# Performance work log

Hardware: AMD Instinct MI355X
Metric: run time of the kernel (lower is better)

Reference implementation:

```python
import jax, jax.numpy as jnp
import numpy as np

E = 500000
B = 1024
N_INC = 64
E_INC = 64
U_INC = 64
W_INC = 2
DIM_IN = E_INC + 2 * N_INC + U_INC          # 256
DIM_W2 = DIM_IN // 2                         # 128
DIM_X1 = DIM_IN + DIM_W2                     # 384
H1 = 256
H2 = 256
E_OUTC = 64
EPS = 1e-5


def _linear_params(key, d_in, d_out):
    kw, kb = jax.random.split(key)
    lim = 1.0 / np.sqrt(d_in)
    W = jax.random.uniform(kw, (d_in, d_out), minval=-lim, maxval=lim, dtype=jnp.float32)
    b = jax.random.uniform(kb, (d_out,), minval=-lim, maxval=lim, dtype=jnp.float32)
    return W, b


def setup_inputs() -> dict:
    key = jax.random.key(0)
    ks = jax.random.split(key, 12)
    src = jax.random.normal(ks[0], (E, N_INC), dtype=jnp.float32)
    dest = jax.random.normal(ks[1], (E, N_INC), dtype=jnp.float32)
    edge_attr = jax.random.normal(ks[2], (E, E_INC), dtype=jnp.float32)
    u = jax.random.normal(ks[3], (B, U_INC), dtype=jnp.float32)
    batch = jax.random.randint(ks[4], (E,), 0, B, dtype=jnp.int64)
    winding = jax.random.uniform(ks[5], (E, W_INC), dtype=jnp.float32)

    Ww, bw = _linear_params(ks[6], W_INC, DIM_W2)
    gw = jnp.ones((DIM_W2,), jnp.float32)
    betaw = jnp.zeros((DIM_W2,), jnp.float32)

    W1, b1 = _linear_params(ks[7], DIM_X1, H1)
    g1 = jnp.ones((H1,), jnp.float32)
    beta1 = jnp.zeros((H1,), jnp.float32)
    W2, b2 = _linear_params(ks[8], H1, H2)
    g2 = jnp.ones((H2,), jnp.float32)
    beta2 = jnp.zeros((H2,), jnp.float32)
    W3, b3 = _linear_params(ks[9], H2, E_OUTC)

    return {
        "src": src, "dest": dest, "edge_attr": edge_attr, "u": u,
        "batch": batch, "winding": winding,
        "Ww": Ww, "bw": bw, "gw": gw, "betaw": betaw,
        "W1": W1, "b1": b1, "g1": g1, "beta1": beta1,
        "W2": W2, "b2": b2, "g2": g2, "beta2": beta2,
        "W3": W3, "b3": b3,
    }


def _layernorm(x, g, b):
    mu = jnp.mean(x, axis=-1, keepdims=True)
    var = jnp.mean(jnp.square(x - mu), axis=-1, keepdims=True)
    return (x - mu) * jax.lax.rsqrt(var + EPS) * g + b


def reference(src, dest, edge_attr, u, batch, winding,
              Ww, bw, gw, betaw,
              W1, b1, g1, beta1,
              W2, b2, g2, beta2,
              W3, b3):
    # winding_mlp: Linear -> LayerNorm -> ReLU, [E, 2] -> [E, 128]
    w = jax.nn.relu(_layernorm(winding @ Ww + bw, gw, betaw))
    # gather per-graph features and concat: [E, 384]
    x = jnp.concatenate([src, dest, edge_attr, u[batch], w], axis=1)
    # mlp_h: (Linear -> LN -> ReLU) x2 -> Linear
    h = jax.nn.relu(_layernorm(x @ W1 + b1, g1, beta1))
    h = jax.nn.relu(_layernorm(h @ W2 + b2, g2, beta2))
    return h @ W3 + b3
```

## Files before the change

### kernel.cpp

```cpp
#include <hip/hip_runtime.h>
#include <stdint.h>

#define E_TOT 500000
#define BM 128
#define NTHREADS 512

typedef float f32x4 __attribute__((ext_vector_type(4)));
typedef short short8 __attribute__((ext_vector_type(8)));

__device__ __forceinline__ float b2f(ushort u) {
    union { uint32_t i; float f; } v; v.i = ((uint32_t)u) << 16; return v.f;
}
__device__ __forceinline__ ushort f2b(float f) {
    union { float f; uint32_t i; } v; v.f = f;
    uint32_t r = (v.i + 0x7FFFu + ((v.i >> 16) & 1u)) >> 16;
    return (ushort)r;
}
__device__ __forceinline__ float ldf(const void* p, int i, int f32m) {
    return f32m ? ((const float*)p)[i] : b2f(((const ushort*)p)[i]);
}

__global__ void detect_fmt(const void* src, const void* batch, int* flags) {
    __shared__ int s_ok, s_nz;
    if (threadIdx.x == 0) { s_ok = 0; s_nz = 0; }
    __syncthreads();
    int t = threadIdx.x;
    if (t < 64) {
        float f = fabsf(b2f(((const ushort*)src)[2 * t]));
        if (f > 1e-3f && f < 1e2f) atomicAdd(&s_ok, 1);
    }
    int hv = ((const int*)batch)[2 * t + 1];
    if (hv != 0) atomicOr(&s_nz, 1);
    __syncthreads();
    if (t == 0) { flags[0] = (s_ok < 32) ? 1 : 0; flags[1] = (s_nz == 0) ? 1 : 0; }
}

__global__ void prep(const int* __restrict__ flags,
                     const void* W1, const void* W2, const void* W3,
                     const void* Ww, const void* bw, const void* gw, const void* bew,
                     const void* b1, const void* g1, const void* be1,
                     const void* b2, const void* g2, const void* be2, const void* b3,
                     ushort* __restrict__ W1t, ushort* __restrict__ W2t,
                     ushort* __restrict__ W3t, float* __restrict__ params) {
    int f32m = flags[0];
    int id = blockIdx.x * 256 + threadIdx.x;
    if (id < 98304) {
        int n = id / 384, k = id - n * 384;
        W1t[id] = f2b(ldf(W1, k * 256 + n, f32m));
    } else if (id < 163840) {
        int t = id - 98304; int n = t >> 8, k = t & 255;
        W2t[t] = f2b(ldf(W2, k * 256 + n, f32m));
    } else if (id < 180224) {
        int t = id - 163840; int n = t >> 8, k = t & 255;
        W3t[t] = f2b(ldf(W3, k * 64 + n, f32m));
    } else if (id < 182464) {
        int p = id - 180224;
        const void* sp; int off;
        if      (p < 256)  { sp = Ww;  off = p; }
        else if (p < 384)  { sp = bw;  off = p - 256; }
        else if (p < 512)  { sp = gw;  off = p - 384; }
        else if (p < 640)  { sp = bew; off = p - 512; }
        else if (p < 896)  { sp = b1;  off = p - 640; }
        else if (p < 1152) { sp = g1;  off = p - 896; }
        else if (p < 1408) { sp = be1; off = p - 1152; }
        else if (p < 1664) { sp = b2;  off = p - 1408; }
        else if (p < 1920) { sp = g2;  off = p - 1664; }
        else if (p < 2176) { sp = be2; off = p - 1920; }
        else               { sp = b3;  off = p - 2176; }
        params[p] = ldf(sp, off, f32m);
    }
}

__global__ __launch_bounds__(NTHREADS, 2) void fused_edge_mlp(
    const void* __restrict__ srcv, const void* __restrict__ destv,
    const void* __restrict__ eav, const void* __restrict__ uv,
    const int* __restrict__ bp, const void* __restrict__ windv,
    const int* __restrict__ flags, const float* __restrict__ params,
    const ushort* __restrict__ W1t, const ushort* __restrict__ W2t, const ushort* __restrict__ W3t,
    float* __restrict__ outp)
{
    __shared__ float s_ww0[128], s_ww1[128], s_bw[128], s_gw[128], s_bew[128];
    __shared__ float s_b1[256], s_g1[256], s_be1[256];
    __shared__ float s_b2[256], s_g2[256], s_be2[256];
    __shared__ float s_b3[64];
    __shared__ int   s_uoff[BM];
    __shared__ __align__(16) ushort wtile[BM * 136];
    __shared__ __align__(16) ushort Ast[BM * 40];
    __shared__ __align__(16) ushort Bst[256 * 40];
    __shared__ __align__(16) ushort htile[BM * 264];
    __shared__ float s_red1[BM * 4], s_red2[BM * 4];
    __shared__ float s_mu[BM], s_rs[BM];

    const int tid  = threadIdx.x;
    const int base = blockIdx.x * BM;
    const int f32m = flags[0];
    const int i64m = flags[1];

    if (tid < 128) {
        s_ww0[tid] = params[tid];        s_ww1[tid] = params[128 + tid];
        s_bw[tid]  = params[256 + tid];  s_gw[tid]  = params[384 + tid];
        s_bew[tid] = params[512 + tid];
        int gr = base + tid; if (gr >= E_TOT) gr = E_TOT - 1;
        int bi = i64m ? bp[2 * gr] : bp[gr];
        s_uoff[tid] = bi * 64;
    } else if (tid < 384) {
        int j = tid - 128;
        s_b1[j] = params[640 + j];  s_g1[j] = params[896 + j];  s_be1[j] = params[1152 + j];
        s_b2[j] = params[1408 + j]; s_g2[j] = params[1664 + j]; s_be2[j] = params[1920 + j];
    } else if (tid < 448) {
        s_b3[tid - 384] = params[2176 + tid - 384];
    }
    __syncthreads();

    {
        int r = tid >> 2, sub = tid & 3;
        int gr = base + r; if (gr >= E_TOT) gr = E_TOT - 1;
        float w0, w1;
        if (f32m) { const float* wp = (const float*)windv; w0 = wp[(long)gr * 2]; w1 = wp[(long)gr * 2 + 1]; }
        else      { const ushort* wp = (const ushort*)windv; w0 = b2f(wp[(long)gr * 2]); w1 = b2f(wp[(long)gr * 2 + 1]); }
        float s1 = 0.f, s2 = 0.f;
        float vv[32];
        #pragma unroll
        for (int j0 = 0; j0 < 32; ++j0) {
            int j = sub * 32 + j0;
            float t = fmaf(w0, s_ww0[j], fmaf(w1, s_ww1[j], s_bw[j]));
            vv[j0] = t; s1 += t; s2 += t * t;
        }
        s1 += __shfl_xor(s1, 1); s2 += __shfl_xor(s2, 1);
        s1 += __shfl_xor(s1, 2); s2 += __shfl_xor(s2, 2);
        float mu  = s1 * (1.f / 128.f);
        float var = s2 * (1.f / 128.f) - mu * mu;
        float rs  = rsqrtf(var + 1e-5f);
        #pragma unroll
        for (int j0 = 0; j0 < 32; ++j0) {
            int j = sub * 32 + j0;
            float t = (vv[j0] - mu) * rs * s_gw[j] + s_bew[j];
            wtile[r * 136 + j] = f2b(fmaxf(t, 0.f));
        }
    }

    const int lane = tid & 63;
    const int wav  = tid >> 6;
    const int q    = lane >> 4, n16 = lane & 15;
    const int rh   = wav >> 2,  cq  = wav & 3;
    const int rowbase = rh * 64, colbase = cq * 64;

    const int st_row = tid >> 2, st_c8 = (tid & 3) * 8;
    int st_gr = base + st_row; if (st_gr >= E_TOT) st_gr = E_TOT - 1;
    const int bn = tid >> 1, bc = (tid & 1) * 16;

    f32x4 acc[4][4];
    #pragma unroll
    for (int a = 0; a < 4; ++a)
        #pragma unroll
        for (int b = 0; b < 4; ++b) acc[a][b] = (f32x4){0.f, 0.f, 0.f, 0.f};

    for (int kc = 0; kc < 12; ++kc) {
        __syncthreads();
        {
            const ushort* g = W1t + bn * 384 + kc * 32 + bc;
            uint4 x0 = *(const uint4*)g;
            uint4 x1 = *(const uint4*)(g + 8);
            *(uint4*)&Bst[bn * 40 + bc]     = x0;
            *(uint4*)&Bst[bn * 40 + bc + 8] = x1;
        }
        if (kc < 8) {
            int grp = kc >> 1, off = (kc & 1) * 32 + st_c8;
            const void* bsrc; long eoff;
            if      (grp == 0) { bsrc = srcv;  eoff = (long)st_gr * 64 + off; }
            else if (grp == 1) { bsrc = destv; eoff = (long)st_gr * 64 + off; }
            else if (grp == 2) { bsrc = eav;   eoff = (long)st_gr * 64 + off; }
            else               { bsrc = uv;    eoff = (long)s_uoff[st_row] + off; }
            uint4 val;
            if (f32m) {
                const float* g = (const float*)bsrc + eoff;
                float4 x0 = *(const float4*)g, x1 = *(const float4*)(g + 4);
                union { uint4 u; ushort s[8]; } pk;
                pk.s[0] = f2b(x0.x); pk.s[1] = f2b(x0.y); pk.s[2] = f2b(x0.z); pk.s[3] = f2b(x0.w);
                pk.s[4] = f2b(x1.x); pk.s[5] = f2b(x1.y); pk.s[6] = f2b(x1.z); pk.s[7] = f2b(x1.w);
                val = pk.u;
            } else {
                val = *(const uint4*)((const ushort*)bsrc + eoff);
            }
            *(uint4*)&Ast[st_row * 40 + st_c8] = val;
        }
        __syncthreads();
        short8 afr[4], bfr[4];
        if (kc < 8) {
            #pragma unroll
            for (int rt = 0; rt < 4; ++rt)
                afr[rt] = *(const short8*)&Ast[(rowbase + rt * 16 + n16) * 40 + q * 8];
        } else {
            #pragma unroll
            for (int rt = 0; rt < 4; ++rt)
                afr[rt] = *(const short8*)&wtile[(rowbase + rt * 16 + n16) * 136 + (kc - 8) * 32 + q * 8];
        }
        #pragma unroll
        for (int ct = 0; ct < 4; ++ct)
            bfr[ct] = *(const short8*)&Bst[(colbase + ct * 16 + n16) * 40 + q * 8];
        #pragma unroll
        for (int rt = 0; rt < 4; ++rt)
            #pragma unroll
            for (int ct = 0; ct < 4; ++ct)
                acc[rt][ct] = __builtin_amdgcn_mfma_f32_16x16x32_bf16(afr[rt], bfr[ct], acc[rt][ct], 0, 0, 0);
    }

    auto ln_epilogue = [&](const float* bias, const float* gamma, const float* beta) {
        #pragma unroll
        for (int rt = 0; rt < 4; ++rt) {
            #pragma unroll
            for (int i = 0; i < 4; ++i) {
                float sv = 0.f, sq = 0.f;
                #pragma unroll
                for (int ct = 0; ct < 4; ++ct) {
                    float t = acc[rt][ct][i] + bias[colbase + ct * 16 + n16];
                    sv += t; sq += t * t;
                }
                #pragma unroll
                for (int m = 1; m < 16; m <<= 1) {
                    sv += __shfl_xor(sv, m); sq += __shfl_xor(sq, m);
                }
                if (n16 == 0) {
                    int row = rowbase + rt * 16 + q * 4 + i;
                    s_red1[row * 4 + cq] = sv; s_red2[row * 4 + cq] = sq;
                }
            }
        }
        __syncthreads();
        if (tid < BM) {
            float sv = s_red1[tid * 4] + s_red1[tid * 4 + 1] + s_red1[tid * 4 + 2] + s_red1[tid * 4 + 3];
            float sq = s_red2[tid * 4] + s_red2[tid * 4 + 1] + s_red2[tid * 4 + 2] + s_red2[tid * 4 + 3];
            float mu  = sv * (1.f / 256.f);
            float var = sq * (1.f / 256.f) - mu * mu;
            s_mu[tid] = mu; s_rs[tid] = rsqrtf(var + 1e-5f);
        }
        __syncthreads();
        #pragma unroll
        for (int rt = 0; rt < 4; ++rt) {
            #pragma unroll
            for (int ct = 0; ct < 4; ++ct) {
                int col = colbase + ct * 16 + n16;
                float bb = bias[col], gg = gamma[col], be = beta[col];
                #pragma unroll
                for (int i = 0; i < 4; ++i) {
                    int row = rowbase + rt * 16 + q * 4 + i;
                    float t = acc[rt][ct][i] + bb;
                    t = (t - s_mu[row]) * s_rs[row] * gg + be;
                    htile[row * 264 + col] = f2b(fmaxf(t, 0.f));
                }
            }
        }
        __syncthreads();
    };
    ln_epilogue(s_b1, s_g1, s_be1);

    #pragma unroll
    for (int a = 0; a < 4; ++a)
        #pragma unroll
        for (int b = 0; b < 4; ++b) acc[a][b] = (f32x4){0.f, 0.f, 0.f, 0.f};
    for (int kc = 0; kc < 8; ++kc) {
        __syncthreads();
        {
            const ushort* g = W2t + bn * 256 + kc * 32 + bc;
            uint4 x0 = *(const uint4*)g;
            uint4 x1 = *(const uint4*)(g + 8);
            *(uint4*)&Bst[bn * 40 + bc]     = x0;
            *(uint4*)&Bst[bn * 40 + bc + 8] = x1;
        }
        __syncthreads();
        short8 afr[4], bfr[4];
        #pragma unroll
        for (int rt = 0; rt < 4; ++rt)
            afr[rt] = *(const short8*)&htile[(rowbase + rt * 16 + n16) * 264 + kc * 32 + q * 8];
        #pragma unroll
        for (int ct = 0; ct < 4; ++ct)
            bfr[ct] = *(const short8*)&Bst[(colbase + ct * 16 + n16) * 40 + q * 8];
        #pragma unroll
        for (int rt = 0; rt < 4; ++rt)
            #pragma unroll
            for (int ct = 0; ct < 4; ++ct)
                acc[rt][ct] = __builtin_amdgcn_mfma_f32_16x16x32_bf16(afr[rt], bfr[ct], acc[rt][ct], 0, 0, 0);
    }
    ln_epilogue(s_b2, s_g2, s_be2);

    f32x4 acc3[4];
    #pragma unroll
    for (int ct = 0; ct < 4; ++ct) acc3[ct] = (f32x4){0.f, 0.f, 0.f, 0.f};
    const int row3 = wav * 16;
    for (int kc = 0; kc < 8; ++kc) {
        __syncthreads();
        if (tid < 128) {
            int n = tid >> 1, c = (tid & 1) * 16;
            const ushort* g = W3t + n * 256 + kc * 32 + c;
            uint4 x0 = *(const uint4*)g;
            uint4 x1 = *(const uint4*)(g + 8);
            *(uint4*)&Bst[n * 40 + c]     = x0;
            *(uint4*)&Bst[n * 40 + c + 8] = x1;
        }
        __syncthreads();
        short8 afr = *(const short8*)&htile[(row3 + n16) * 264 + kc * 32 + q * 8];
        #pragma unroll
        for (int ct = 0; ct < 4; ++ct) {
            short8 bfr = *(const short8*)&Bst[(ct * 16 + n16) * 40 + q * 8];
            acc3[ct] = __builtin_amdgcn_mfma_f32_16x16x32_bf16(afr, bfr, acc3[ct], 0, 0, 0);
        }
    }
    #pragma unroll
    for (int ct = 0; ct < 4; ++ct) {
        int col = ct * 16 + n16;
        float bb = s_b3[col];
        #pragma unroll
        for (int i = 0; i < 4; ++i) {
            int row = row3 + q * 4 + i;
            int gr  = base + row;
            if (gr < E_TOT) outp[(long)gr * 64 + col] = acc3[ct][i] + bb;
        }
    }
}

extern "C" void kernel_launch(void* const* d_in, const int* in_sizes, int n_in,
                              void* d_out, int out_size, void* d_ws, size_t ws_size,
                              hipStream_t stream) {
    int*    flags  = (int*)d_ws;
    float*  params = (float*)((char*)d_ws + 16);
    ushort* W1t    = (ushort*)((char*)d_ws + 9216);
    ushort* W2t    = W1t + 98304;
    ushort* W3t    = W2t + 65536;

    detect_fmt<<<1, 256, 0, stream>>>(d_in[0], d_in[4], flags);
    prep<<<713, 256, 0, stream>>>(flags,
        d_in[10], d_in[14], d_in[18],
        d_in[6], d_in[7], d_in[8], d_in[9],
        d_in[11], d_in[12], d_in[13],
        d_in[15], d_in[16], d_in[17], d_in[19],
        W1t, W2t, W3t, params);

    int nblocks = (E_TOT + BM - 1) / BM;
    fused_edge_mlp<<<nblocks, NTHREADS, 0, stream>>>(
        d_in[0], d_in[1], d_in[2], d_in[3], (const int*)d_in[4], d_in[5],
        flags, params, W1t, W2t, W3t, (float*)d_out);
}
```

Measured before the change: 879.5 us.

## Load MLP fragments directly from global memory and share one swizzled LDS tile

Layer-1 A fragments are now read straight from global memory into MFMA registers, and all weight fragments are loaded from global/L2 per wave, replacing LDS staging and the paired barriers in every k-chunk. The winding and hidden activations share one XOR-swizzled 128x256 LDS buffer to avoid bank conflicts and shrink LDS use. Launch bounds are raised to four blocks per CU, and layer 3 is re-tiled into 2x2 MFMA tiles per wave. Prep now reads the weights coalesced and scatters the transposed writes. The risks are more redundant global and L2 weight traffic, uncoalesced per-lane row loads, and register pressure under the tighter launch bound.

```diff
diff --git a/kernel.cpp b/kernel.cpp
--- a/kernel.cpp
+++ b/kernel.cpp
@@ -45,14 +45,14 @@
     int f32m = flags[0];
     int id = blockIdx.x * 256 + threadIdx.x;
     if (id < 98304) {
-        int n = id / 384, k = id - n * 384;
-        W1t[id] = f2b(ldf(W1, k * 256 + n, f32m));
+        int k = id >> 8, n = id & 255;
+        W1t[n * 384 + k] = f2b(ldf(W1, id, f32m));
     } else if (id < 163840) {
-        int t = id - 98304; int n = t >> 8, k = t & 255;
-        W2t[t] = f2b(ldf(W2, k * 256 + n, f32m));
+        int t = id - 98304; int k = t >> 8, n = t & 255;
+        W2t[n * 256 + k] = f2b(ldf(W2, t, f32m));
     } else if (id < 180224) {
-        int t = id - 163840; int n = t >> 8, k = t & 255;
-        W3t[t] = f2b(ldf(W3, k * 64 + n, f32m));
+        int t = id - 163840; int k = t >> 6, n = t & 63;
+        W3t[n * 256 + k] = f2b(ldf(W3, t, f32m));
     } else if (id < 182464) {
         int p = id - 180224;
         const void* sp; int off;
@@ -71,7 +71,7 @@
     }
 }
 
-__global__ __launch_bounds__(NTHREADS, 2) void fused_edge_mlp(
+__global__ __launch_bounds__(NTHREADS, 4) void fused_edge_mlp(
     const void* __restrict__ srcv, const void* __restrict__ destv,
     const void* __restrict__ eav, const void* __restrict__ uv,
     const int* __restrict__ bp, const void* __restrict__ windv,
@@ -79,15 +79,12 @@
     const ushort* __restrict__ W1t, const ushort* __restrict__ W2t, const ushort* __restrict__ W3t,
     float* __restrict__ outp)
 {
+    __shared__ __align__(16) ushort xh[BM * 256];
     __shared__ float s_ww0[128], s_ww1[128], s_bw[128], s_gw[128], s_bew[128];
     __shared__ float s_b1[256], s_g1[256], s_be1[256];
     __shared__ float s_b2[256], s_g2[256], s_be2[256];
     __shared__ float s_b3[64];
     __shared__ int   s_uoff[BM];
-    __shared__ __align__(16) ushort wtile[BM * 136];
-    __shared__ __align__(16) ushort Ast[BM * 40];
-    __shared__ __align__(16) ushort Bst[256 * 40];
-    __shared__ __align__(16) ushort htile[BM * 264];
     __shared__ float s_red1[BM * 4], s_red2[BM * 4];
     __shared__ float s_mu[BM], s_rs[BM];
 
@@ -135,19 +132,31 @@
         for (int j0 = 0; j0 < 32; ++j0) {
             int j = sub * 32 + j0;
             float t = (vv[j0] - mu) * rs * s_gw[j] + s_bew[j];
-            wtile[r * 136 + j] = f2b(fmaxf(t, 0.f));
-        }
-    }
+            xh[r * 256 + ((((j >> 3) ^ (r & 7))) << 3) + (j & 7)] = f2b(fmaxf(t, 0.f));
+        }
+    }
+    __syncthreads();
 
     const int lane = tid & 63;
     const int wav  = tid >> 6;
     const int q    = lane >> 4, n16 = lane & 15;
     const int rh   = wav >> 2,  cq  = wav & 3;
     const int rowbase = rh * 64, colbase = cq * 64;
-
-    const int st_row = tid >> 2, st_c8 = (tid & 3) * 8;
-    int st_gr = base + st_row; if (st_gr >= E_TOT) st_gr = E_TOT - 1;
-    const int bn = tid >> 1, bc = (tid & 1) * 16;
+    const int koff = q * 8;
+
+    int rowA[4], grA[4], uofA[4];
+    #pragma unroll
+    for (int rt = 0; rt < 4; ++rt) {
+        int row = rowbase + rt * 16 + n16;
+        rowA[rt] = row;
+        int gr = base + row; if (gr >= E_TOT) gr = E_TOT - 1;
+        grA[rt] = gr;
+        uofA[rt] = s_uoff[row];
+    }
+
+    auto xh_frag = [&](int row, int colg) -> short8 {
+        return *(const short8*)&xh[row * 256 + ((colg ^ (row & 7)) << 3)];
+    };
 
     f32x4 acc[4][4];
     #pragma unroll
@@ -155,49 +164,67 @@
         #pragma unroll
         for (int b = 0; b < 4; ++b) acc[a][b] = (f32x4){0.f, 0.f, 0.f, 0.f};
 
-    for (int kc = 0; kc < 12; ++kc) {
-        __syncthreads();
-        {
-            const ushort* g = W1t + bn * 384 + kc * 32 + bc;
-            uint4 x0 = *(const uint4*)g;
-            uint4 x1 = *(const uint4*)(g + 8);
-            *(uint4*)&Bst[bn * 40 + bc]     = x0;
-            *(uint4*)&Bst[bn * 40 + bc + 8] = x1;
-        }
-        if (kc < 8) {
-            int grp = kc >> 1, off = (kc & 1) * 32 + st_c8;
-            const void* bsrc; long eoff;
-            if      (grp == 0) { bsrc = srcv;  eoff = (long)st_gr * 64 + off; }
-            else if (grp == 1) { bsrc = destv; eoff = (long)st_gr * 64 + off; }
-            else if (grp == 2) { bsrc = eav;   eoff = (long)st_gr * 64 + off; }
-            else               { bsrc = uv;    eoff = (long)s_uoff[st_row] + off; }
-            uint4 val;
-            if (f32m) {
-                const float* g = (const float*)bsrc + eoff;
-                float4 x0 = *(const float4*)g, x1 = *(const float4*)(g + 4);
-                union { uint4 u; ushort s[8]; } pk;
+    const ushort* w1p[4];
+    #pragma unroll
+    for (int ct = 0; ct < 4; ++ct)
+        w1p[ct] = W1t + (colbase + ct * 16 + n16) * 384 + koff;
+
+    if (!f32m) {
+        #pragma unroll
+        for (int kc = 0; kc < 8; ++kc) {
+            const int grp = kc >> 1, off = (kc & 1) * 32 + koff;
+            short8 afr[4], bfr[4];
+            #pragma unroll
+            for (int rt = 0; rt < 4; ++rt) {
+                const ushort* ap;
+                if      (grp == 0) ap = (const ushort*)srcv  + (long)grA[rt] * 64 + off;
+                else if (grp == 1) ap = (const ushort*)destv + (long)grA[rt] * 64 + off;
+                else if (grp == 2) ap = (const ushort*)eav   + (long)grA[rt] * 64 + off;
+                else               ap = (const ushort*)uv    + uofA[rt] + off;
+                afr[rt] = *(const short8*)ap;
+            }
+            #pragma unroll
+            for (int ct = 0; ct < 4; ++ct) bfr[ct] = *(const short8*)(w1p[ct] + kc * 32);
+            #pragma unroll
+            for (int rt = 0; rt < 4; ++rt)
+                #pragma unroll
+                for (int ct = 0; ct < 4; ++ct)
+                    acc[rt][ct] = __builtin_amdgcn_mfma_f32_16x16x32_bf16(afr[rt], bfr[ct], acc[rt][ct], 0, 0, 0);
+        }
+    } else {
+        #pragma unroll
+        for (int kc = 0; kc < 8; ++kc) {
+            const int grp = kc >> 1, off = (kc & 1) * 32 + koff;
+            short8 afr[4], bfr[4];
+            #pragma unroll
+            for (int rt = 0; rt < 4; ++rt) {
+                const float* ap;
+                if      (grp == 0) ap = (const float*)srcv  + (long)grA[rt] * 64 + off;
+                else if (grp == 1) ap = (const float*)destv + (long)grA[rt] * 64 + off;
+                else if (grp == 2) ap = (const float*)eav   + (long)grA[rt] * 64 + off;
+                else               ap = (const float*)uv    + uofA[rt] + off;
+                float4 x0 = *(const float4*)ap, x1 = *(const float4*)(ap + 4);
+                union { short8 v; ushort s[8]; } pk;
                 pk.s[0] = f2b(x0.x); pk.s[1] = f2b(x0.y); pk.s[2] = f2b(x0.z); pk.s[3] = f2b(x0.w);
                 pk.s[4] = f2b(x1.x); pk.s[5] = f2b(x1.y); pk.s[6] = f2b(x1.z); pk.s[7] = f2b(x1.w);
-                val = pk.u;
-            } else {
-                val = *(const uint4*)((const ushort*)bsrc + eoff);
-            }
-            *(uint4*)&Ast[st_row * 40 + st_c8] = val;
-        }
-        __syncthreads();
+                afr[rt] = pk.v;
+            }
+            #pragma unroll
+            for (int ct = 0; ct < 4; ++ct) bfr[ct] = *(const short8*)(w1p[ct] + kc * 32);
+            #pragma unroll
+            for (int rt = 0; rt < 4; ++rt)
+                #pragma unroll
+                for (int ct = 0; ct < 4; ++ct)
+                    acc[rt][ct] = __builtin_amdgcn_mfma_f32_16x16x32_bf16(afr[rt], bfr[ct], acc[rt][ct], 0, 0, 0);
+        }
+    }
+    #pragma unroll
+    for (int kc = 8; kc < 12; ++kc) {
         short8 afr[4], bfr[4];
-        if (kc < 8) {
-            #pragma unroll
-            for (int rt = 0; rt < 4; ++rt)
-                afr[rt] = *(const short8*)&Ast[(rowbase + rt * 16 + n16) * 40 + q * 8];
-        } else {
-            #pragma unroll
-            for (int rt = 0; rt < 4; ++rt)
-                afr[rt] = *(const short8*)&wtile[(rowbase + rt * 16 + n16) * 136 + (kc - 8) * 32 + q * 8];
-        }
-        #pragma unroll
-        for (int ct = 0; ct < 4; ++ct)
-            bfr[ct] = *(const short8*)&Bst[(colbase + ct * 16 + n16) * 40 + q * 8];
+        #pragma unroll
+        for (int rt = 0; rt < 4; ++rt) afr[rt] = xh_frag(rowA[rt], (kc - 8) * 4 + q);
+        #pragma unroll
+        for (int ct = 0; ct < 4; ++ct) bfr[ct] = *(const short8*)(w1p[ct] + kc * 32);
         #pragma unroll
         for (int rt = 0; rt < 4; ++rt)
             #pragma unroll
@@ -246,7 +273,7 @@
                     int row = rowbase + rt * 16 + q * 4 + i;
                     float t = acc[rt][ct][i] + bb;
                     t = (t - s_mu[row]) * s_rs[row] * gg + be;
-                    htile[row * 264 + col] = f2b(fmaxf(t, 0.f));
+                    xh[row * 256 + ((((col >> 3) ^ (row & 7))) << 3) + (col & 7)] = f2b(fmaxf(t, 0.f));
                 }
             }
         }
@@ -258,23 +285,17 @@
     for (int a = 0; a < 4; ++a)
         #pragma unroll
         for (int b = 0; b < 4; ++b) acc[a][b] = (f32x4){0.f, 0.f, 0.f, 0.f};
+    const ushort* w2p[4];
+    #pragma unroll
+    for (int ct = 0; ct < 4; ++ct)
+        w2p[ct] = W2t + (colbase + ct * 16 + n16) * 256 + koff;
+    #pragma unroll
     for (int kc = 0; kc < 8; ++kc) {
-        __syncthreads();
-        {
-            const ushort* g = W2t + bn * 256 + kc * 32 + bc;
-            uint4 x0 = *(const uint4*)g;
-            uint4 x1 = *(const uint4*)(g + 8);
-            *(uint4*)&Bst[bn * 40 + bc]     = x0;
-            *(uint4*)&Bst[bn * 40 + bc + 8] = x1;
-        }
-        __syncthreads();
         short8 afr[4], bfr[4];
         #pragma unroll
-        for (int rt = 0; rt < 4; ++rt)
-            afr[rt] = *(const short8*)&htile[(rowbase + rt * 16 + n16) * 264 + kc * 32 + q * 8];
-        #pragma unroll
-        for (int ct = 0; ct < 4; ++ct)
-            bfr[ct] = *(const short8*)&Bst[(colbase + ct * 16 + n16) * 40 + q * 8];
+        for (int rt = 0; rt < 4; ++rt) afr[rt] = xh_frag(rowA[rt], kc * 4 + q);
+        #pragma unroll
+        for (int ct = 0; ct < 4; ++ct) bfr[ct] = *(const short8*)(w2p[ct] + kc * 32);
         #pragma unroll
         for (int rt = 0; rt < 4; ++rt)
             #pragma unroll
@@ -283,37 +304,44 @@
     }
     ln_epilogue(s_b2, s_g2, s_be2);
 
-    f32x4 acc3[4];
-    #pragma unroll
-    for (int ct = 0; ct < 4; ++ct) acc3[ct] = (f32x4){0.f, 0.f, 0.f, 0.f};
-    const int row3 = wav * 16;
+    f32x4 acc3[2][2];
+    #pragma unroll
+    for (int a = 0; a < 2; ++a)
+        #pragma unroll
+        for (int b = 0; b < 2; ++b) acc3[a][b] = (f32x4){0.f, 0.f, 0.f, 0.f};
+    const int rgrp = wav >> 1, chalf = wav & 1;
+    int row3[2];
+    #pragma unroll
+    for (int rt = 0; rt < 2; ++rt) row3[rt] = rgrp * 32 + rt * 16 + n16;
+    const ushort* w3p[2];
+    #pragma unroll
+    for (int ct = 0; ct < 2; ++ct)
+        w3p[ct] = W3t + (chalf * 32 + ct * 16 + n16) * 256 + koff;
+    #pragma unroll
     for (int kc = 0; kc < 8; ++kc) {
-        __syncthreads();
-        if (tid < 128) {
-            int n = tid >> 1, c = (tid & 1) * 16;
-            const ushort* g = W3t + n * 256 + kc * 32 + c;
-            uint4 x0 = *(const uint4*)g;
-            uint4 x1 = *(const uint4*)(g + 8);
-            *(uint4*)&Bst[n * 40 + c]     = x0;
-            *(uint4*)&Bst[n * 40 + c + 8] = x1;
-        }
-        __syncthreads();
-        short8 afr = *(const short8*)&htile[(row3 + n16) * 264 + kc * 32 + q * 8];
-        #pragma unroll
-        for (int ct = 0; ct < 4; ++ct) {
-            short8 bfr = *(const short8*)&Bst[(ct * 16 + n16) * 40 + q * 8];
-            acc3[ct] = __builtin_amdgcn_mfma_f32_16x16x32_bf16(afr, bfr, acc3[ct], 0, 0, 0);
-        }
-    }
-    #pragma unroll
-    for (int ct = 0; ct < 4; ++ct) {
-        int col = ct * 16 + n16;
-        float bb = s_b3[col];
-        #pragma unroll
-        for (int i = 0; i < 4; ++i) {
-            int row = row3 + q * 4 + i;
-            int gr  = base + row;
-            if (gr < E_TOT) outp[(long)gr * 64 + col] = acc3[ct][i] + bb;
+        short8 a3[2], b3r[2];
+        #pragma unroll
+        for (int rt = 0; rt < 2; ++rt) a3[rt] = xh_frag(row3[rt], kc * 4 + q);
+        #pragma unroll
+        for (int ct = 0; ct < 2; ++ct) b3r[ct] = *(const short8*)(w3p[ct] + kc * 32);
+        #pragma unroll
+        for (int rt = 0; rt < 2; ++rt)
+            #pragma unroll
+            for (int ct = 0; ct < 2; ++ct)
+                acc3[rt][ct] = __builtin_amdgcn_mfma_f32_16x16x32_bf16(a3[rt], b3r[ct], acc3[rt][ct], 0, 0, 0);
+    }
+    #pragma unroll
+    for (int rt = 0; rt < 2; ++rt) {
+        #pragma unroll
+        for (int ct = 0; ct < 2; ++ct) {
+            int col = chalf * 32 + ct * 16 + n16;
+            float bb = s_b3[col];
+            #pragma unroll
+            for (int i = 0; i < 4; ++i) {
+                int row = rgrp * 32 + rt * 16 + q * 4 + i;
+                int gr  = base + row;
+                if (gr < E_TOT) outp[(long)gr * 64 + col] = acc3[rt][ct][i] + bb;
+            }
         }
     }
 }
```

After: 1.295 ms. +47.2%, slower.
